# Optimization experiments

Hardware: AMD Instinct MI355X
Metric: run time of the kernel (lower is better)

## Reference

```python
import jax, jax.numpy as jnp
import numpy as np

S = 2048      # total tokens
DIM = 1024    # model dim
H = 16        # attention heads
DH = 64       # head dim
BOT = 256     # bottleneck dim
NIMG = 4      # images (equal size)
L = S // NIMG # tokens per image
K = 256       # sparse_k
IH = 4        # indexer heads
ID = 16       # indexer head dim
MAXREL = 64   # hardcoded in module
NBUCK = 2 * MAXREL + 1
GH = IH * 2   # gate MLP hidden (expansion=2)


def setup_inputs() -> dict:
    key = jax.random.key(0)
    ks = jax.random.split(key, 16)
    r = lambda i, sh, s=0.02: jax.random.normal(ks[i], sh, jnp.float32) * s
    return dict(
        hidden_states=jax.random.normal(ks[0], (S, DIM), jnp.float32),
        patch_coords=jax.random.randint(ks[1], (S, 2), 0, 64, dtype=jnp.int32),
        cu_seqlens=jnp.arange(NIMG + 1, dtype=jnp.int32) * L,
        rotary_pos_emb=jax.random.uniform(ks[2], (S, DH // 2), jnp.float32) * 3.0,
        Wq_idx=r(3, (2 * IH * ID, DIM)),
        Wk_idx=r(4, (2 * IH * ID, DIM)),
        W1g=r(5, (GH, IH)), b1g=jnp.zeros((GH,), jnp.float32),
        W2g=r(6, (IH, GH)), b2g=jnp.zeros((IH,), jnp.float32),
        rpe_table=r(7, (NBUCK, IH)),
        Wqkv_d=r(8, (BOT, DIM)), bqkv_d=jnp.zeros((BOT,), jnp.float32),
        Wqkv_u=r(9, (3 * DIM, BOT)), bqkv_u=jnp.zeros((3 * DIM,), jnp.float32),
        Wp_d=r(10, (BOT, DIM)), bp_d=jnp.zeros((BOT,), jnp.float32),
        Wp_u=r(11, (DIM, BOT)), bp_u=jnp.zeros((DIM,), jnp.float32),
        scaler=jnp.ones((1,), jnp.float32),
    )


def _rotate_half(x):
    x1, x2 = jnp.split(x, 2, axis=-1)
    return jnp.concatenate([-x2, x1], axis=-1)


def reference(hidden_states, patch_coords, cu_seqlens, rotary_pos_emb,
              Wq_idx, Wk_idx, W1g, b1g, W2g, b2g, rpe_table,
              Wqkv_d, bqkv_d, Wqkv_u, bqkv_u, Wp_d, bp_d, Wp_u, bp_u, scaler):
    n = cu_seqlens.shape[0] - 1            # images (equal size L)
    Li = hidden_states.shape[0] // n
    neg = jnp.finfo(hidden_states.dtype).min

    # QKV via low-rank bottleneck
    qkv = (hidden_states @ Wqkv_d.T + bqkv_d) @ Wqkv_u.T + bqkv_u  # [S, 3*DIM]
    qkv = qkv.reshape(S, 3, H, DH)
    q, k, v = qkv[:, 0], qkv[:, 1], qkv[:, 2]                      # [S, H, DH]

    # vision RoPE (emb = cat(rpe, rpe))
    emb = jnp.concatenate([rotary_pos_emb, rotary_pos_emb], axis=-1)  # [S, DH]
    cos = jnp.cos(emb)[:, None, :]
    sin = jnpp if False else jnp.sin(emb)[:, None, :]
    q = q * cos + _rotate_half(q) * sin
    k = k * cos + _rotate_half(k) * sin

    # ---- interaction indexer, vmapped over equal-size images ----
    xs = hidden_states.reshape(n, Li, DIM)
    pos = patch_coords[:, 1].reshape(n, Li).astype(jnp.float32)
    qI = (xs @ Wq_idx.T).reshape(n, Li, 2 * IH, ID)
    kI = (xs @ Wk_idx.T).reshape(n, Li, 2 * IH, ID)
    dot = jnp.einsum('nqhd,nkhd->nqkh', qI, kI)                    # [n, L, L, 2*IH]
    data_in, gate_in = dot[..., :IH], dot[..., IH:]
    rel = jnp.clip(pos[:, :, None] - pos[:, None, :], -MAXREL, MAXREL)
    bucket = (rel + MAXREL).astype(jnp.int32)                      # [n, L, L]
    rpe = rpe_table[bucket]                                        # [n, L, L, IH]
    relu_scores = jax.nn.relu(data_in + rpe)
    g = jax.nn.sigmoid(jax.nn.relu((gate_in + rpe) @ W1g.T + b1g) @ W2g.T + b2g)
    index_scores = (relu_scores * g).sum(-1)                       # [n, L, L]

    # top-k sparse mask (0 at selected keys, -inf-ish elsewhere)
    _, topk_idx = jax.lax.top_k(index_scores, K)                   # [n, L, K]
    ni = jnp.arange(n)[:, None, None]
    ri = jnp.arange(Li)[None, :, None]
    mask_local = jnp.full((n, Li, Li), neg, hidden_states.dtype).at[ni, ri, topk_idx].set(0.0)

    # block-diagonal full mask
    mask = jnp.full((S, S), neg, hidden_states.dtype)
    for i in range(n):
        mask = mask.at[i * Li:(i + 1) * Li, i * Li:(i + 1) * Li].set(mask_local[i])

    # dense SDPA with additive mask
    att = jnp.einsum('qhd,khd->hqk', q, k) / jnp.sqrt(jnp.float32(DH)).astype(q.dtype)
    att = att + mask[None]
    p = jax.nn.softmax(att, axis=-1)
    out = jnp.einsum('hqk,khd->qhd', p, v).reshape(S, H * DH)

    final = (out @ Wp_d.T + bp_d) @ Wp_u.T + bp_u
    return final * scaler
```

## Files before the change

### kernel.cpp

```cpp
#include <hip/hip_runtime.h>
#include <hip/hip_bf16.h>

#define S_    2048
#define DIM_  1024
#define H_    16
#define DH_   64
#define BOT_  256
#define NIMG_ 4
#define LI_   512
#define K_    256
#define IH_   4
#define ID_   16
#define MAXREL_ 64
#define NBUCK_ 129
#define GH_   8
#define IDH2_ 128

typedef short bf16x8 __attribute__((ext_vector_type(8)));
typedef float f32x4  __attribute__((ext_vector_type(4)));

__device__ __forceinline__ unsigned short f2bf(float x) {
    unsigned u = __float_as_uint(x);
    return (unsigned short)((u + 0x7fffu + ((u >> 16) & 1u)) >> 16);
}
__device__ __forceinline__ float bf2f(unsigned short h) {
    return __uint_as_float(((unsigned)h) << 16);
}

#define OFF_W1_    2097152
#define OFF_WQ_    2359296
#define OFF_WK_    2490368
#define OFF_WQKVU_ 2621440
#define OFF_WPD_   3407872
#define OFF_WPU_   3670016
#define NSPLIT_    3932160

__global__ __launch_bounds__(256) void split_all_kernel(
    const float* __restrict__ hid, const float* __restrict__ wqd,
    const float* __restrict__ wq,  const float* __restrict__ wk,
    const float* __restrict__ wqu, const float* __restrict__ wpd,
    const float* __restrict__ wpu,
    unsigned short* __restrict__ hi, unsigned short* __restrict__ lo)
{
    long e = ((long)blockIdx.x * 256 + threadIdx.x) * 4;
    if (e >= NSPLIT_) return;
    const float* src; long off;
    if (e < OFF_W1_)         { src = hid; off = 0; }
    else if (e < OFF_WQ_)    { src = wqd; off = OFF_W1_; }
    else if (e < OFF_WK_)    { src = wq;  off = OFF_WQ_; }
    else if (e < OFF_WQKVU_) { src = wk;  off = OFF_WK_; }
    else if (e < OFF_WPD_)   { src = wqu; off = OFF_WQKVU_; }
    else if (e < OFF_WPU_)   { src = wpd; off = OFF_WPD_; }
    else                     { src = wpu; off = OFF_WPU_; }
    float4 v = *(const float4*)(src + (e - off));
    ushort4 h, l;
    h.x = f2bf(v.x); l.x = f2bf(v.x - bf2f(h.x));
    h.y = f2bf(v.y); l.y = f2bf(v.y - bf2f(h.y));
    h.z = f2bf(v.z); l.z = f2bf(v.z - bf2f(h.z));
    h.w = f2bf(v.w); l.w = f2bf(v.w - bf2f(h.w));
    *(ushort4*)&hi[e] = h;
    *(ushort4*)&lo[e] = l;
}

__global__ __launch_bounds__(256) void gemm_bf16x3(
    const unsigned short* __restrict__ Ah, const unsigned short* __restrict__ Al,
    const unsigned short* __restrict__ Bh, const unsigned short* __restrict__ Bl,
    const float* __restrict__ bias, const float* __restrict__ scale_ptr,
    float* __restrict__ Cf, int M, int N, int Kd)
{
    __shared__ unsigned short sAh[128 * 40], sAl[128 * 40];
    __shared__ unsigned short sBh[64 * 40],  sBl[64 * 40];
    int tid = threadIdx.x;
    int lane = tid & 63, wv = tid >> 6;
    int wr = wv >> 1, wc = wv & 1;
    int row0 = blockIdx.y * 128, col0 = blockIdx.x * 64;

    f32x4 acc[4][2];
#pragma unroll
    for (int i = 0; i < 4; i++)
#pragma unroll
        for (int j = 0; j < 2; j++) acc[i][j] = (f32x4){0.f, 0.f, 0.f, 0.f};

    int ar = tid >> 1, ac = (tid & 1) * 16;
    int br = tid >> 2, bc = (tid & 3) * 8;
    const unsigned short* gAh = Ah + (size_t)(row0 + ar) * Kd + ac;
    const unsigned short* gAl = Al + (size_t)(row0 + ar) * Kd + ac;
    const unsigned short* gBh = Bh + (size_t)(col0 + br) * Kd + bc;
    const unsigned short* gBl = Bl + (size_t)(col0 + br) * Kd + bc;
    int am = lane & 15, qk = (lane >> 4) * 8;

    for (int k0 = 0; k0 < Kd; k0 += 32) {
        __syncthreads();
        *(float4*)&sAh[ar * 40 + ac]     = *(const float4*)(gAh + k0);
        *(float4*)&sAh[ar * 40 + ac + 8] = *(const float4*)(gAh + k0 + 8);
        *(float4*)&sAl[ar * 40 + ac]     = *(const float4*)(gAl + k0);
        *(float4*)&sAl[ar * 40 + ac + 8] = *(const float4*)(gAl + k0 + 8);
        *(float4*)&sBh[br * 40 + bc]     = *(const float4*)(gBh + k0);
        *(float4*)&sBl[br * 40 + bc]     = *(const float4*)(gBl + k0);
        __syncthreads();

        bf16x8 ah[4], al[4], bh[2], bl[2];
#pragma unroll
        for (int rt = 0; rt < 4; rt++) {
            int r = wr * 64 + rt * 16 + am;
            ah[rt] = *(const bf16x8*)&sAh[r * 40 + qk];
            al[rt] = *(const bf16x8*)&sAl[r * 40 + qk];
        }
#pragma unroll
        for (int ct = 0; ct < 2; ct++) {
            int c = wc * 32 + ct * 16 + am;
            bh[ct] = *(const bf16x8*)&sBh[c * 40 + qk];
            bl[ct] = *(const bf16x8*)&sBl[c * 40 + qk];
        }
#pragma unroll
        for (int rt = 0; rt < 4; rt++)
#pragma unroll
            for (int ct = 0; ct < 2; ct++) {
                acc[rt][ct] = __builtin_amdgcn_mfma_f32_16x16x32_bf16(ah[rt], bh[ct], acc[rt][ct], 0, 0, 0);
                acc[rt][ct] = __builtin_amdgcn_mfma_f32_16x16x32_bf16(ah[rt], bl[ct], acc[rt][ct], 0, 0, 0);
                acc[rt][ct] = __builtin_amdgcn_mfma_f32_16x16x32_bf16(al[rt], bh[ct], acc[rt][ct], 0, 0, 0);
            }
    }

    float scl = scale_ptr ? *scale_ptr : 1.0f;
    int rq = (lane >> 4) * 4;
#pragma unroll
    for (int rt = 0; rt < 4; rt++)
#pragma unroll
        for (int ct = 0; ct < 2; ct++) {
            int col = col0 + wc * 32 + ct * 16 + am;
            float bz = bias ? bias[col] : 0.0f;
#pragma unroll
            for (int rg = 0; rg < 4; rg++) {
                int row = row0 + wr * 64 + rt * 16 + rq + rg;
                Cf[(size_t)row * N + col] = (acc[rt][ct][rg] + bz) * scl;
            }
        }
}

__global__ __launch_bounds__(256) void gemm64_bf16x3(
    const unsigned short* __restrict__ Ah, const unsigned short* __restrict__ Al,
    const unsigned short* __restrict__ Bh, const unsigned short* __restrict__ Bl,
    const float* __restrict__ bias_lo, const float* __restrict__ bias_hi,
    float* __restrict__ Cf, unsigned short* __restrict__ Chi,
    unsigned short* __restrict__ Clo, int M, int N, int Kd, int split_col)
{
    __shared__ unsigned short sAh[64 * 72], sAl[64 * 72];
    __shared__ unsigned short sBh[64 * 72], sBl[64 * 72];
    int tid = threadIdx.x;
    int lane = tid & 63, wv = tid >> 6;
    int wr = wv >> 1, wc = wv & 1;
    int row0 = blockIdx.y * 64, col0 = blockIdx.x * 64;

    f32x4 acc[2][2];
#pragma unroll
    for (int i = 0; i < 2; i++)
#pragma unroll
        for (int j = 0; j < 2; j++) acc[i][j] = (f32x4){0.f, 0.f, 0.f, 0.f};

    int sr = tid >> 2, sc = (tid & 3) * 16;
    const unsigned short* gAh = Ah + (size_t)(row0 + sr) * Kd + sc;
    const unsigned short* gAl = Al + (size_t)(row0 + sr) * Kd + sc;
    const unsigned short* gBh = Bh + (size_t)(col0 + sr) * Kd + sc;
    const unsigned short* gBl = Bl + (size_t)(col0 + sr) * Kd + sc;
    int am = lane & 15, qk = (lane >> 4) * 8;

    for (int k0 = 0; k0 < Kd; k0 += 64) {
        __syncthreads();
        *(float4*)&sAh[sr * 72 + sc]     = *(const float4*)(gAh + k0);
        *(float4*)&sAh[sr * 72 + sc + 8] = *(const float4*)(gAh + k0 + 8);
        *(float4*)&sAl[sr * 72 + sc]     = *(const float4*)(gAl + k0);
        *(float4*)&sAl[sr * 72 + sc + 8] = *(const float4*)(gAl + k0 + 8);
        *(float4*)&sBh[sr * 72 + sc]     = *(const float4*)(gBh + k0);
        *(float4*)&sBh[sr * 72 + sc + 8] = *(const float4*)(gBh + k0 + 8);
        *(float4*)&sBl[sr * 72 + sc]     = *(const float4*)(gBl + k0);
        *(float4*)&sBl[sr * 72 + sc + 8] = *(const float4*)(gBl + k0 + 8);
        __syncthreads();

#pragma unroll
        for (int ks = 0; ks < 2; ks++) {
            bf16x8 ah[2], al[2], bh[2], bl[2];
#pragma unroll
            for (int rt = 0; rt < 2; rt++) {
                int r = wr * 32 + rt * 16 + am;
                ah[rt] = *(const bf16x8*)&sAh[r * 72 + ks * 32 + qk];
                al[rt] = *(const bf16x8*)&sAl[r * 72 + ks * 32 + qk];
            }
#pragma unroll
            for (int ct = 0; ct < 2; ct++) {
                int c = wc * 32 + ct * 16 + am;
                bh[ct] = *(const bf16x8*)&sBh[c * 72 + ks * 32 + qk];
                bl[ct] = *(const bf16x8*)&sBl[c * 72 + ks * 32 + qk];
            }
#pragma unroll
            for (int rt = 0; rt < 2; rt++)
#pragma unroll
                for (int ct = 0; ct < 2; ct++) {
                    acc[rt][ct] = __builtin_amdgcn_mfma_f32_16x16x32_bf16(ah[rt], bh[ct], acc[rt][ct], 0, 0, 0);
                    acc[rt][ct] = __builtin_amdgcn_mfma_f32_16x16x32_bf16(ah[rt], bl[ct], acc[rt][ct], 0, 0, 0);
                    acc[rt][ct] = __builtin_amdgcn_mfma_f32_16x16x32_bf16(al[rt], bh[ct], acc[rt][ct], 0, 0, 0);
                }
        }
    }

    int rq = (lane >> 4) * 4;
#pragma unroll
    for (int rt = 0; rt < 2; rt++)
#pragma unroll
        for (int ct = 0; ct < 2; ct++) {
            int col = col0 + wc * 32 + ct * 16 + am;
#pragma unroll
            for (int rg = 0; rg < 4; rg++) {
                int row = row0 + wr * 32 + rt * 16 + rq + rg;
                float v = acc[rt][ct][rg];
                if (col < split_col) {
                    if (bias_lo) v += bias_lo[col];
                    size_t idx = (size_t)row * split_col + col;
                    unsigned short hh = f2bf(v);
                    Chi[idx] = hh;
                    Clo[idx] = f2bf(v - bf2f(hh));
                } else {
                    if (bias_hi) v += bias_hi[col - split_col];
                    Cf[(size_t)row * (N - split_col) + col - split_col] = v;
                }
            }
        }
}

__global__ __launch_bounds__(256) void ropesplit_kernel(
    const float* __restrict__ qkv, const float* __restrict__ rope,
    unsigned short* __restrict__ qkvh, unsigned short* __restrict__ qkvl)
{
    int idx = blockIdx.x * 256 + threadIdx.x;
    int d = idx & 63;
    int hh = (idx >> 6) & (H_ - 1);
    int s = idx >> 10;
    size_t base = (size_t)s * 3072 + hh * 64 + d;
    float q = qkv[base];
    float k = qkv[base + 1024];
    float v = qkv[base + 2048];
    float r = rope[s * 32 + (d & 31)];
    float c = cosf(r), sn = sinf(r);
    float qp = __shfl_xor(q, 32, 64);
    float kp = __shfl_xor(k, 32, 64);
    float sgn = (d < 32) ? -1.0f : 1.0f;
    float qr = (q * c + sgn * qp * sn) * 0.125f;
    float kr = k * c + sgn * kp * sn;
    unsigned short h1 = f2bf(qr);
    qkvh[base] = h1;            qkvl[base] = f2bf(qr - bf2f(h1));
    unsigned short h2 = f2bf(kr);
    qkvh[base + 1024] = h2;     qkvl[base + 1024] = f2bf(kr - bf2f(h2));
    unsigned short h3 = f2bf(v);
    qkvh[base + 2048] = h3;     qkvl[base + 2048] = f2bf(v - bf2f(h3));
}

__global__ __launch_bounds__(256) void score_topk_kernel(
    const float* __restrict__ qIk,
    const int* __restrict__ coords, const float* __restrict__ rpe_table,
    const float* __restrict__ W1g, const float* __restrict__ b1g,
    const float* __restrict__ W2g, const float* __restrict__ b2g,
    unsigned* __restrict__ selmask)
{
    __shared__ float skI[64][132];
    __shared__ float sqI2[4][IDH2_];
    __shared__ unsigned skeys[4][LI_];
    __shared__ int shist[4][256];
    __shared__ float srpe[NBUCK_ * IH_];
    __shared__ float sW1[GH_ * IH_], sb1[GH_], sW2[IH_ * GH_], sb2[IH_];

    int tid  = threadIdx.x;
    int lane = tid & 63;
    int wv   = tid >> 6;
    int row  = blockIdx.x * 4 + wv;
    int n    = (blockIdx.x * 4) >> 9;

    for (int i = tid; i < NBUCK_ * IH_; i += 256) srpe[i] = rpe_table[i];
    if (tid < 32) sW1[tid] = W1g[tid];
    else if (tid < 64) sW2[tid - 32] = W2g[tid - 32];
    else if (tid < 72) sb1[tid - 64] = b1g[tid - 64];
    else if (tid < 76) sb2[tid - 72] = b2g[tid - 72];
    for (int i = tid; i < 4 * IDH2_; i += 256)
        sqI2[i >> 7][i & 127] =
            qIk[(size_t)(blockIdx.x * 4 + (i >> 7)) * 256 + (i & 127)];
    int pq = coords[row * 2 + 1];

    for (int kt = 0; kt < 8; kt++) {
        __syncthreads();
        {
            int r  = tid >> 2;
            int d0 = (tid & 3) * 32;
            const float* src = qIk + (size_t)(n * LI_ + kt * 64 + r) * 256 + 128 + d0;
#pragma unroll
            for (int j = 0; j < 8; j++)
                *(float4*)&skI[r][d0 + j * 4] = *(const float4*)(src + j * 4);
        }
        __syncthreads();

        int kloc = lane;
        int kg   = kt * 64 + kloc;
        const float* sq = &sqI2[wv][0];
        float dh[8];
#pragma unroll
        for (int hh = 0; hh < 8; hh++) {
            float acc = 0.0f;
#pragma unroll
            for (int d = 0; d < 16; d += 4) {
                float4 kv = *(const float4*)&skI[kloc][hh * 16 + d];
                acc += sq[hh * 16 + d + 0] * kv.x + sq[hh * 16 + d + 1] * kv.y +
                       sq[hh * 16 + d + 2] * kv.z + sq[hh * 16 + d + 3] * kv.w;
            }
            dh[hh] = acc;
        }
        int pk = coords[(n * LI_ + kg) * 2 + 1];
        int rel = pq - pk;
        rel = rel < -MAXREL_ ? -MAXREL_ : (rel > MAXREL_ ? MAXREL_ : rel);
        const float* rp = srpe + (rel + MAXREL_) * IH_;
        float t1[GH_];
#pragma unroll
        for (int g = 0; g < GH_; g++) t1[g] = sb1[g];
#pragma unroll
        for (int j = 0; j < IH_; j++) {
            float gate = dh[IH_ + j] + rp[j];
#pragma unroll
            for (int g = 0; g < GH_; g++) t1[g] += gate * sW1[g * IH_ + j];
        }
#pragma unroll
        for (int g = 0; g < GH_; g++) t1[g] = fmaxf(t1[g], 0.0f);
        float score = 0.0f;
#pragma unroll
        for (int j = 0; j < IH_; j++) {
            float t2 = sb2[j];
#pragma unroll
            for (int g = 0; g < GH_; g++) t2 += t1[g] * sW2[j * GH_ + g];
            float sg = 1.0f / (1.0f + expf(-t2));
            float rs = fmaxf(dh[j] + rp[j], 0.0f);
            score += rs * sg;
        }
        unsigned bits = __float_as_uint(score);
        skeys[wv][kg] = (bits & 0x80000000u) ? ~bits : (bits | 0x80000000u);
    }

    unsigned pref = 0u;
    int kcur = K_;
    const unsigned himask[4] = {0u, 0xFF000000u, 0xFFFF0000u, 0xFFFFFF00u};
#pragma unroll
    for (int pass = 0; pass < 4; pass++) {
        int shift = 24 - pass * 8;
        unsigned hm = himask[pass];
        *(int4*)&shist[wv][4 * lane] = make_int4(0, 0, 0, 0);
#pragma unroll
        for (int c = 0; c < 8; c++) {
            unsigned key = skeys[wv][c * 64 + lane];
            if ((key & hm) == pref) atomicAdd(&shist[wv][(key >> shift) & 255], 1);
        }
        int4 b4 = *(const int4*)&shist[wv][4 * lane];
        int b[4] = {b4.x, b4.y, b4.z, b4.w};
        int t = b[0] + b[1] + b[2] + b[3];
        int Ssum = t;
#pragma unroll
        for (int off = 1; off < 64; off <<= 1) {
            int u = __shfl_down(Ssum, off, 64);
            if (lane + off < 64) Ssum += u;
        }
        int E = Ssum - t;
        int cs[5];
        cs[4] = E;
        cs[3] = b[3] + E;
        cs[2] = b[2] + cs[3];
        cs[1] = b[1] + cs[2];
        cs[0] = b[0] + cs[1];
        bool found = false;
        unsigned cpref = 0u; int ck = 0;
#pragma unroll
        for (int j = 0; j < 4; j++) {
            if (!found && cs[j] >= kcur && cs[j + 1] < kcur) {
                found = true;
                cpref = pref | ((unsigned)(4 * lane + j) << shift);
                ck = kcur - cs[j + 1];
            }
        }
        unsigned long long bm = __ballot(found);
        int src = __ffsll((long long)bm) - 1;
        pref = (unsigned)__shfl((int)cpref, src, 64);
        kcur = __shfl(ck, src, 64);
    }
    unsigned Tu = pref;

    unsigned long long bg[8], be[8];
#pragma unroll
    for (int c = 0; c < 8; c++) {
        unsigned key = skeys[wv][c * 64 + lane];
        bg[c] = __ballot(key > Tu);
        be[c] = __ballot(key == Tu);
    }
    if (lane < 16) {
        int total_gt = 0;
#pragma unroll
        for (int c = 0; c < 8; c++) total_gt += __popcll(bg[c]);
        int base = 0;
#pragma unroll
        for (int c = 0; c < 8; c++) {
            if (2 * c < lane)     base += __popc((unsigned)be[c]);
            if (2 * c + 1 < lane) base += __popc((unsigned)(be[c] >> 32));
        }
        unsigned gw = (unsigned)(bg[lane >> 1] >> (32 * (lane & 1)));
        unsigned ew = (unsigned)(be[lane >> 1] >> (32 * (lane & 1)));
        int ne = K_ - total_gt - base;
        int pc = __popc(ew);
        int m = ne < 0 ? 0 : (ne > pc ? pc : ne);
        while (pc > m) { ew ^= (1u << (31 - __clz(ew))); pc--; }
        selmask[(size_t)row * 16 + lane] = gw | ew;
    }
}

__global__ __launch_bounds__(256) void attn_kernel(
    const unsigned short* __restrict__ qkvh, const unsigned short* __restrict__ qkvl,
    const unsigned* __restrict__ selmask,
    unsigned short* __restrict__ outh, unsigned short* __restrict__ outl)
{
    __shared__ unsigned short Qh[64 * 72],  Ql[64 * 72];
    __shared__ unsigned short Kh[64 * 72],  Kl[64 * 72];
    __shared__ unsigned short VTh[64 * 72], VTl[64 * 72];
    __shared__ unsigned short Ph[64 * 72],  Pl[64 * 72];
    __shared__ unsigned Ms[64][16];

    int b  = blockIdx.x;
    int qt = b >> 6;
    int nh = b & 63;
    int h  = nh & 15;
    int n  = nh >> 4;
    int tid = threadIdx.x;
    int lane = tid & 63, w = tid >> 6;
    int lane15 = lane & 15, quad = lane >> 4;
    int q0 = n * LI_ + qt * 64;

    for (int i = tid; i < 64 * 16; i += 256)
        Ms[i >> 4][i & 15] = selmask[(size_t)(q0 + (i >> 4)) * 16 + (i & 15)];

    {
        int r = tid >> 2, c0 = (tid & 3) * 16;
        size_t off = (size_t)(q0 + r) * 3072 + h * 64 + c0;
        *(uint4*)&Qh[r * 72 + c0]     = *(const uint4*)(qkvh + off);
        *(uint4*)&Qh[r * 72 + c0 + 8] = *(const uint4*)(qkvh + off + 8);
        *(uint4*)&Ql[r * 72 + c0]     = *(const uint4*)(qkvl + off);
        *(uint4*)&Ql[r * 72 + c0 + 8] = *(const uint4*)(qkvl + off + 8);
    }
    __syncthreads();
    bf16x8 qfh[2], qfl[2];
#pragma unroll
    for (int ks = 0; ks < 2; ks++) {
        qfh[ks] = *(const bf16x8*)&Qh[(16 * w + lane15) * 72 + ks * 32 + quad * 8];
        qfl[ks] = *(const bf16x8*)&Ql[(16 * w + lane15) * 72 + ks * 32 + quad * 8];
    }

    f32x4 o_acc[4];
#pragma unroll
    for (int i = 0; i < 4; i++) o_acc[i] = (f32x4){0.f, 0.f, 0.f, 0.f};
    float rsum[4] = {};

    for (int kt = 0; kt < 8; kt++) {
        __syncthreads();
        {
            int r = tid >> 2, c0 = (tid & 3) * 16;
            size_t off = (size_t)(n * LI_ + kt * 64 + r) * 3072 + 1024 + h * 64 + c0;
            *(uint4*)&Kh[r * 72 + c0]     = *(const uint4*)(qkvh + off);
            *(uint4*)&Kh[r * 72 + c0 + 8] = *(const uint4*)(qkvh + off + 8);
            *(uint4*)&Kl[r * 72 + c0]     = *(const uint4*)(qkvl + off);
            *(uint4*)&Kl[r * 72 + c0 + 8] = *(const uint4*)(qkvl + off + 8);
        }
        {
            int dd = lane;
            int k0 = w * 16;
            size_t off = (size_t)(n * LI_ + kt * 64 + k0) * 3072 + 2048 + h * 64 + dd;
            unsigned short hb[16], lb[16];
#pragma unroll
            for (int j = 0; j < 16; j++) {
                hb[j] = qkvh[off + (size_t)j * 3072];
                lb[j] = qkvl[off + (size_t)j * 3072];
            }
            *(uint4*)&VTh[dd * 72 + k0]     = *(uint4*)&hb[0];
            *(uint4*)&VTh[dd * 72 + k0 + 8] = *(uint4*)&hb[8];
            *(uint4*)&VTl[dd * 72 + k0]     = *(uint4*)&lb[0];
            *(uint4*)&VTl[dd * 72 + k0 + 8] = *(uint4*)&lb[8];
        }
        __syncthreads();

        f32x4 s_acc[4];
#pragma unroll
        for (int nt = 0; nt < 4; nt++) s_acc[nt] = (f32x4){0.f, 0.f, 0.f, 0.f};
        __builtin_amdgcn_s_setprio(1);
#pragma unroll
        for (int nt = 0; nt < 4; nt++) {
#pragma unroll
            for (int ks = 0; ks < 2; ks++) {
                bf16x8 kfh = *(const bf16x8*)&Kh[(16 * nt + lane15) * 72 + ks * 32 + quad * 8];
                bf16x8 kfl = *(const bf16x8*)&Kl[(16 * nt + lane15) * 72 + ks * 32 + quad * 8];
                s_acc[nt] = __builtin_amdgcn_mfma_f32_16x16x32_bf16(qfh[ks], kfh, s_acc[nt], 0, 0, 0);
                s_acc[nt] = __builtin_amdgcn_mfma_f32_16x16x32_bf16(qfh[ks], kfl, s_acc[nt], 0, 0, 0);
                s_acc[nt] = __builtin_amdgcn_mfma_f32_16x16x32_bf16(qfl[ks], kfh, s_acc[nt], 0, 0, 0);
            }
        }
        __builtin_amdgcn_s_setprio(0);

#pragma unroll
        for (int nt = 0; nt < 4; nt++) {
            int kb = kt * 64 + nt * 16 + lane15;
            int wi = kb >> 5, bit = kb & 31;
#pragma unroll
            for (int reg = 0; reg < 4; reg++) {
                int qloc = 16 * w + quad * 4 + reg;
                unsigned mw = Ms[qloc][wi];
                float p = ((mw >> bit) & 1u) ? __expf(s_acc[nt][reg]) : 0.0f;
                rsum[reg] += p;
                unsigned short ph = f2bf(p);
                Ph[qloc * 72 + nt * 16 + lane15] = ph;
                Pl[qloc * 72 + nt * 16 + lane15] = f2bf(p - bf2f(ph));
            }
        }

        {
            bf16x8 pfh[2], pfl[2];
#pragma unroll
            for (int ks = 0; ks < 2; ks++) {
                pfh[ks] = *(const bf16x8*)&Ph[(16 * w + lane15) * 72 + ks * 32 + quad * 8];
                pfl[ks] = *(const bf16x8*)&Pl[(16 * w + lane15) * 72 + ks * 32 + quad * 8];
            }
            __builtin_amdgcn_s_setprio(1);
#pragma unroll
            for (int dt = 0; dt < 4; dt++) {
#pragma unroll
                for (int ks = 0; ks < 2; ks++) {
                    bf16x8 vfh = *(const bf16x8*)&VTh[(16 * dt + lane15) * 72 + ks * 32 + quad * 8];
                    bf16x8 vfl = *(const bf16x8*)&VTl[(16 * dt + lane15) * 72 + ks * 32 + quad * 8];
                    o_acc[dt] = __builtin_amdgcn_mfma_f32_16x16x32_bf16(pfh[ks], vfh, o_acc[dt], 0, 0, 0);
                    o_acc[dt] = __builtin_amdgcn_mfma_f32_16x16x32_bf16(pfh[ks], vfl, o_acc[dt], 0, 0, 0);
                    o_acc[dt] = __builtin_amdgcn_mfma_f32_16x16x32_bf16(pfl[ks], vfh, o_acc[dt], 0, 0, 0);
                }
            }
            __builtin_amdgcn_s_setprio(0);
        }
    }

#pragma unroll
    for (int reg = 0; reg < 4; reg++) {
        rsum[reg] += __shfl_xor(rsum[reg], 1, 64);
        rsum[reg] += __shfl_xor(rsum[reg], 2, 64);
        rsum[reg] += __shfl_xor(rsum[reg], 4, 64);
        rsum[reg] += __shfl_xor(rsum[reg], 8, 64);
    }

#pragma unroll
    for (int dt = 0; dt < 4; dt++) {
#pragma unroll
        for (int reg = 0; reg < 4; reg++) {
            float v = o_acc[dt][reg] / rsum[reg];
            size_t ob = (size_t)(q0 + 16 * w + quad * 4 + reg) * 1024 + h * 64 + 16 * dt + lane15;
            unsigned short hh = f2bf(v);
            outh[ob] = hh;
            outl[ob] = f2bf(v - bf2f(hh));
        }
    }
}

extern "C" void kernel_launch(void* const* d_in, const int* in_sizes, int n_in,
                              void* d_out, int out_size, void* d_ws, size_t ws_size,
                              hipStream_t stream)
{
    const float* hidden  = (const float*)d_in[0];
    const int*   coords  = (const int*)d_in[1];
    const float* rope    = (const float*)d_in[3];
    const float* Wq_idx  = (const float*)d_in[4];
    const float* Wk_idx  = (const float*)d_in[5];
    const float* W1g     = (const float*)d_in[6];
    const float* b1g     = (const float*)d_in[7];
    const float* W2g     = (const float*)d_in[8];
    const float* b2g     = (const float*)d_in[9];
    const float* rpe     = (const float*)d_in[10];
    const float* Wqkv_d  = (const float*)d_in[11];
    const float* bqkv_d  = (const float*)d_in[12];
    const float* Wqkv_u  = (const float*)d_in[13];
    const float* bqkv_u  = (const float*)d_in[14];
    const float* Wp_d    = (const float*)d_in[15];
    const float* bp_d    = (const float*)d_in[16];
    const float* Wp_u    = (const float*)d_in[17];
    const float* bp_u    = (const float*)d_in[18];
    const float* scaler  = (const float*)d_in[19];
    float* out = (float*)d_out;

    unsigned short* sp_hi  = (unsigned short*)d_ws;
    unsigned short* sp_lo  = sp_hi + NSPLIT_;
    unsigned short* mid_hi = sp_lo + NSPLIT_;
    unsigned short* mid_lo = mid_hi + (size_t)S_ * BOT_;
    float* qkv = (float*)(mid_lo + (size_t)S_ * BOT_);
    float* qIk = qkv + (size_t)S_ * 3 * DIM_;
    unsigned* selmask = (unsigned*)(qIk + (size_t)S_ * 256);
    unsigned short* qkvh = (unsigned short*)(selmask + (size_t)S_ * 16);
    unsigned short* qkvl = qkvh + (size_t)S_ * 3 * DIM_;

    split_all_kernel<<<(NSPLIT_ / 4 + 255) / 256, 256, 0, stream>>>(
        hidden, Wqkv_d, Wq_idx, Wk_idx, Wqkv_u, Wp_d, Wp_u, sp_hi, sp_lo);

    gemm64_bf16x3<<<dim3(512 / 64, S_ / 64), 256, 0, stream>>>(
        sp_hi, sp_lo, sp_hi + OFF_W1_, sp_lo + OFF_W1_,
        bqkv_d, nullptr, qIk, mid_hi, mid_lo, S_, 512, DIM_, 256);

    score_topk_kernel<<<S_ / 4, 256, 0, stream>>>(
        qIk, coords, rpe, W1g, b1g, W2g, b2g, selmask);

    gemm_bf16x3<<<dim3(3 * DIM_ / 64, S_ / 128), 256, 0, stream>>>(
        mid_hi, mid_lo, sp_hi + OFF_WQKVU_, sp_lo + OFF_WQKVU_,
        bqkv_u, nullptr, qkv, S_, 3 * DIM_, BOT_);

    ropesplit_kernel<<<(S_ * H_ * 64) / 256, 256, 0, stream>>>(
        qkv, rope, qkvh, qkvl);

    attn_kernel<<<NIMG_ * H_ * 8, 256, 0, stream>>>(qkvh, qkvl, selmask, sp_hi, sp_lo);

    gemm64_bf16x3<<<dim3(BOT_ / 64, S_ / 64), 256, 0, stream>>>(
        sp_hi, sp_lo, sp_hi + OFF_WPD_, sp_lo + OFF_WPD_,
        bp_d, nullptr, nullptr, mid_hi, mid_lo, S_, BOT_, DIM_, BOT_);

    gemm_bf16x3<<<dim3(DIM_ / 64, S_ / 128), 256, 0, stream>>>(
        mid_hi, mid_lo, sp_hi + OFF_WPU_, sp_lo + OFF_WPU_,
        bp_u, scaler, out, S_, DIM_, BOT_);
}
```

Before: 250.1 us.

## Split score_topk per-row work across two waves and lane halves

```diff
diff --git a/kernel.cpp b/kernel.cpp
--- a/kernel.cpp
+++ b/kernel.cpp
@@ -262,27 +262,32 @@
     unsigned* __restrict__ selmask)
 {
     __shared__ float skI[64][132];
-    __shared__ float sqI2[4][IDH2_];
-    __shared__ unsigned skeys[4][LI_];
+    __shared__ float sqI2[2][IDH2_];
+    __shared__ unsigned skeys[2][LI_];
     __shared__ int shist[4][256];
     __shared__ float srpe[NBUCK_ * IH_];
     __shared__ float sW1[GH_ * IH_], sb1[GH_], sW2[IH_ * GH_], sb2[IH_];
 
     int tid  = threadIdx.x;
     int lane = tid & 63;
-    int wv   = tid >> 6;
-    int row  = blockIdx.x * 4 + wv;
-    int n    = (blockIdx.x * 4) >> 9;
+    int w    = tid >> 6;
+    int rw   = w >> 1;
+    int kh   = w & 1;
+    int row  = blockIdx.x * 2 + rw;
+    int n    = (blockIdx.x * 2) >> 9;
 
     for (int i = tid; i < NBUCK_ * IH_; i += 256) srpe[i] = rpe_table[i];
     if (tid < 32) sW1[tid] = W1g[tid];
     else if (tid < 64) sW2[tid - 32] = W2g[tid - 32];
     else if (tid < 72) sb1[tid - 64] = b1g[tid - 64];
     else if (tid < 76) sb2[tid - 72] = b2g[tid - 72];
-    for (int i = tid; i < 4 * IDH2_; i += 256)
+    for (int i = tid; i < 2 * IDH2_; i += 256)
         sqI2[i >> 7][i & 127] =
-            qIk[(size_t)(blockIdx.x * 4 + (i >> 7)) * 256 + (i & 127)];
+            qIk[(size_t)(blockIdx.x * 2 + (i >> 7)) * 256 + (i & 127)];
     int pq = coords[row * 2 + 1];
+
+    int half = lane >> 5, k5 = lane & 31;
+    const float* sq = &sqI2[rw][0];
 
     for (int kt = 0; kt < 8; kt++) {
         __syncthreads();
@@ -296,21 +301,33 @@
         }
         __syncthreads();
 
-        int kloc = lane;
+        int kloc = kh * 32 + k5;
         int kg   = kt * 64 + kloc;
-        const float* sq = &sqI2[wv][0];
+        const float* kp = &skI[kloc][0];
+
+        float dh4[4];
+#pragma unroll
+        for (int hh = 0; hh < 4; hh++) {
+            int h = 4 * half + hh;
+            float acc = 0.0f;
+#pragma unroll
+            for (int dq = 0; dq < 4; dq++) {
+                float4 kv = *(const float4*)(kp + h * 16 + dq * 4);
+                const float* sqp = sq + h * 16 + dq * 4;
+                acc += sqp[0] * kv.x + sqp[1] * kv.y + sqp[2] * kv.z + sqp[3] * kv.w;
+            }
+            dh4[hh] = acc;
+        }
+        float oth[4];
+#pragma unroll
+        for (int j = 0; j < 4; j++) oth[j] = __shfl_xor(dh4[j], 32, 64);
         float dh[8];
 #pragma unroll
-        for (int hh = 0; hh < 8; hh++) {
-            float acc = 0.0f;
-#pragma unroll
-            for (int d = 0; d < 16; d += 4) {
-                float4 kv = *(const float4*)&skI[kloc][hh * 16 + d];
-                acc += sq[hh * 16 + d + 0] * kv.x + sq[hh * 16 + d + 1] * kv.y +
-                       sq[hh * 16 + d + 2] * kv.z + sq[hh * 16 + d + 3] * kv.w;
-            }
-            dh[hh] = acc;
-        }
+        for (int j = 0; j < 4; j++) {
+            dh[j]     = half ? oth[j] : dh4[j];
+            dh[4 + j] = half ? dh4[j] : oth[j];
+        }
+
         int pk = coords[(n * LI_ + kg) * 2 + 1];
         int rel = pq - pk;
         rel = rel < -MAXREL_ ? -MAXREL_ : (rel > MAXREL_ ? MAXREL_ : rel);
@@ -337,8 +354,10 @@
             score += rs * sg;
         }
         unsigned bits = __float_as_uint(score);
-        skeys[wv][kg] = (bits & 0x80000000u) ? ~bits : (bits | 0x80000000u);
-    }
+        unsigned keyv = (bits & 0x80000000u) ? ~bits : (bits | 0x80000000u);
+        if (half == 0) skeys[rw][kg] = keyv;
+    }
+    __syncthreads();
 
     unsigned pref = 0u;
     int kcur = K_;
@@ -347,13 +366,13 @@
     for (int pass = 0; pass < 4; pass++) {
         int shift = 24 - pass * 8;
         unsigned hm = himask[pass];
-        *(int4*)&shist[wv][4 * lane] = make_int4(0, 0, 0, 0);
+        *(int4*)&shist[w][4 * lane] = make_int4(0, 0, 0, 0);
 #pragma unroll
         for (int c = 0; c < 8; c++) {
-            unsigned key = skeys[wv][c * 64 + lane];
-            if ((key & hm) == pref) atomicAdd(&shist[wv][(key >> shift) & 255], 1);
-        }
-        int4 b4 = *(const int4*)&shist[wv][4 * lane];
+            unsigned key = skeys[rw][c * 64 + lane];
+            if ((key & hm) == pref) atomicAdd(&shist[w][(key >> shift) & 255], 1);
+        }
+        int4 b4 = *(const int4*)&shist[w][4 * lane];
         int b[4] = {b4.x, b4.y, b4.z, b4.w};
         int t = b[0] + b[1] + b[2] + b[3];
         int Ssum = t;
@@ -389,11 +408,11 @@
     unsigned long long bg[8], be[8];
 #pragma unroll
     for (int c = 0; c < 8; c++) {
-        unsigned key = skeys[wv][c * 64 + lane];
+        unsigned key = skeys[rw][c * 64 + lane];
         bg[c] = __ballot(key > Tu);
         be[c] = __ballot(key == Tu);
     }
-    if (lane < 16) {
+    if (kh == 0 && lane < 16) {
         int total_gt = 0;
 #pragma unroll
         for (int c = 0; c < 8; c++) total_gt += __popcll(bg[c]);
@@ -604,7 +623,7 @@
         sp_hi, sp_lo, sp_hi + OFF_W1_, sp_lo + OFF_W1_,
         bqkv_d, nullptr, qIk, mid_hi, mid_lo, S_, 512, DIM_, 256);
 
-    score_topk_kernel<<<S_ / 4, 256, 0, stream>>>(
+    score_topk_kernel<<<S_ / 2, 256, 0, stream>>>(
         qIk, coords, rpe, W1g, b1g, W2g, b2g, selmask);
 
     gemm_bf16x3<<<dim3(3 * DIM_ / 64, S_ / 128), 256, 0, stream>>>(
```

Result: slower. 269.1 us (+7.6%).
